# Optimization experiments

Measured on AMD Instinct MI355X. Metric: run time of the kernel, lower is better.

The kernel has to match this reference:

```python
import jax, jax.numpy as jnp
from jax import lax
import numpy as np

DIM = 768      # model dim
NL = 12        # num mamba layers
DS = 16        # d_state
DI = 1536      # d_inner = 2*dim
DC = 4         # d_conv
P = 16         # patch size
IMG = 256
NP = (IMG // P) ** 2  # 256 patches
GS = 5         # KAN grid_size
SO = 3         # KAN spline_order
NK = NL // 3   # 4 KAN layers
BATCH = 32


def setup_inputs() -> dict:
    key = jax.random.key(0)
    ks = jax.random.split(key, 16)
    def n(k, shape, s=0.02):
        return jax.random.normal(k, shape, jnp.float32) * s
    return {
        "x": jax.random.normal(ks[0], (BATCH, 3, IMG, IMG), jnp.float32),
        "patch_w": n(ks[1], (DIM, 3, P, P)),
        "patch_b": jnp.zeros((DIM,), jnp.float32),
        "pos_embed": n(ks[2], (1, NP, DIM)),
        "in_proj_w": n(ks[3], (NL, 2 * DI, DIM)),
        "conv_w": n(ks[4], (NL, DI, 1, DC), 0.1),
        "conv_b": jnp.zeros((NL, DI), jnp.float32),
        "x_proj_w": n(ks[5], (NL, 2 * DS, DI)),
        "dt_proj_w": n(ks[6], (NL, DS, DI)),
        "dt_proj_b": jnp.zeros((NL, DS), jnp.float32),
        "A_log": jnp.tile(jnp.log(jnp.arange(1, DS + 1, dtype=jnp.float32)), (NL, 1)),
        "D_param": jnp.ones((NL, DI), jnp.float32),
        "out_proj_w": n(ks[7], (NL, DIM, DI)),
        "kan_base_w": n(ks[8], (NK, DIM, DIM)),
        "kan_coeff": n(ks[9], (NK, DIM, DIM, GS + SO), 0.1),
        "kan_bias": n(ks[10], (NK, DIM), 0.01),
        "norm_w": jnp.ones((DIM,), jnp.float32),
        "norm_b": jnp.zeros((DIM,), jnp.float32),
    }


def _mamba_block(x, in_w, cw, cb, xpw, dtw, dtb, alog, Dp, ow):
    Bsz, L, _ = x.shape
    xr = jnp.einsum('bld,ed->ble', x, in_w)              # [B,L,2*DI]
    x1, res = xr[..., :DI], xr[..., DI:]
    # causal depthwise conv (pad d_conv-1 on left, truncate to L)
    xc = lax.conv_general_dilated(
        x1.transpose(0, 2, 1), cw, (1,), [(DC - 1, 0)],
        feature_group_count=DI,
        dimension_numbers=('NCH', 'OIH', 'NCH')) + cb[None, :, None]
    x1 = jax.nn.silu(xc.transpose(0, 2, 1))              # [B,L,DI]
    x_dbl = jnp.einsum('bld,ed->ble', x1, xpw)           # [B,L,2*DS]
    Bp = x_dbl[..., DS:]                                 # dt half of x_proj is discarded (as in torch)
    dt = jax.nn.softplus(jnp.einsum('bld,nd->bln', x1, dtw) + dtb)  # [B,L,DS]
    A = -jnp.exp(alog)                                   # [DS]
    Ad = jnp.exp(A * dt)                                 # [B,L,DS]
    u = x1[..., :DI // DS].mean(-1)                      # [B,L]
    Bd = dt * Bp * u[..., None]                          # [B,L,DS]
    def step(s, ab):
        a, b = ab
        s = s * a + b
        return s, s
    _, ys = lax.scan(step, jnp.zeros((Bsz, DS), x.dtype),
                     (Ad.transpose(1, 0, 2), Bd.transpose(1, 0, 2)))
    y = ys.transpose(1, 0, 2)                            # [B,L,DS]
    y = jnp.repeat(y, DI // DS, axis=-1)                 # n -> (n d)
    y = y + x1 * Dp
    y = y * jax.nn.silu(res)
    return jnp.einsum('bld,ed->ble', y, ow)              # [B,L,DIM]


def _kan(xf, bw, coeff, bias):
    base = xf @ bw.T + bias
    grid = jnp.linspace(-1.0, 1.0, GS + 1)
    denom = grid[1:] - grid[:-1] + 1e-8
    xs = (xf[..., None] - grid[:-1]) / denom             # [M,DIM,GS]
    basis = jnp.where((xs >= 0) & (xs < 1), xs, 0.0)
    return base + jnp.einsum('bik,oik->bo', basis, coeff[:, :, :GS])


def reference(x, patch_w, patch_b, pos_embed, in_proj_w, conv_w, conv_b,
              x_proj_w, dt_proj_w, dt_proj_b, A_log, D_param, out_proj_w,
              kan_base_w, kan_coeff, kan_bias, norm_w, norm_b):
    Bsz = x.shape[0]
    h = lax.conv_general_dilated(
        x, patch_w, (P, P), 'VALID',
        dimension_numbers=('NCHW', 'OIHW', 'NCHW')) + patch_b[None, :, None, None]
    h = h.transpose(0, 2, 3, 1).reshape(Bsz, NP, DIM) + pos_embed
    for i in range(NL):
        h = _mamba_block(h, in_proj_w[i], conv_w[i], conv_b[i], x_proj_w[i],
                         dt_proj_w[i], dt_proj_b[i], A_log[i], D_param[i], out_proj_w[i])
        if i % 3 == 2 and i // 3 < NK:
            j = i // 3
            hf = h.reshape(-1, DIM)
            h = _kan(hf, kan_base_w[j], kan_coeff[j], kan_bias[j]).reshape(Bsz, NP, DIM) + h
    mu = h.mean(-1, keepdims=True)
    var = ((h - mu) ** 2).mean(-1, keepdims=True)
    return (h - mu) / jnp.sqrt(var + 1e-5) * norm_w + norm_b
```

## Files before the change

kernel.cpp:

```cpp
#include <hip/hip_runtime.h>

#define BATCH 32
#define NPATCH 256
#define MROWS (BATCH * NPATCH)
#define DIM 768
#define DI 1536
#define DS 16

typedef __bf16 bf16_t;
typedef __attribute__((ext_vector_type(8))) __bf16 bf16x8;
typedef __attribute__((ext_vector_type(4))) float floatx4;

__device__ __forceinline__ float bf2f(unsigned short u) {
    union { unsigned int i; float f; } v; v.i = ((unsigned int)u) << 16; return v.f;
}
__device__ __forceinline__ unsigned short f2bf(float f) {
    union { float f; unsigned int i; } u; u.f = f;
    unsigned int r = u.i + 0x7FFFu + ((u.i >> 16) & 1u);
    return (unsigned short)(r >> 16);
}
__device__ __forceinline__ float ldin(const void* p, int i, int bf) {
    if (bf) return bf2f(((const unsigned short*)p)[i]);
    return ((const float*)p)[i];
}
__device__ __forceinline__ float4 ldin4(const void* p, int i, int bf) {
    if (bf) {
        ushort4 u = *(const ushort4*)((const unsigned short*)p + i);
        return make_float4(bf2f(u.x), bf2f(u.y), bf2f(u.z), bf2f(u.w));
    }
    return *(const float4*)((const float*)p + i);
}
__device__ __forceinline__ float siluf(float x) { return x / (1.0f + expf(-x)); }

__global__ void detect_k(const void* alog, int* flag) {
    if (threadIdx.x == 0 && blockIdx.x == 0) {
        float v = ((const float*)alog)[1];
        flag[0] = (fabsf(v - 0.69314718f) < 0.01f) ? 0 : 1;
    }
}

__global__ __launch_bounds__(256) void cvt4_k(const int* __restrict__ flag,
                                              const void* __restrict__ in,
                                              unsigned short* __restrict__ out, int n4) {
    int i = blockIdx.x * 256 + threadIdx.x;
    if (i >= n4) return;
    float4 v = ldin4(in, i * 4, flag[0]);
    ushort4 o;
    o.x = f2bf(v.x); o.y = f2bf(v.y); o.z = f2bf(v.z); o.w = f2bf(v.w);
    *(ushort4*)(out + i * 4) = o;
}

__global__ __launch_bounds__(256) void kcoef_k(const int* __restrict__ flag,
                                               const void* __restrict__ co,
                                               bf16_t* __restrict__ out) {
    int idx = blockIdx.x * 256 + threadIdx.x;
    int bf = flag[0];
    int j = idx / (768 * 3840);
    int r = idx - j * (768 * 3840);
    int n = r / 3840;
    int kk = r - n * 3840;
    int i = kk / 5, k5 = kk - i * 5;
    out[idx] = (bf16_t)ldin(co, ((j * 768 + n) * 768 + i) * 8 + k5, bf);
}

__global__ __launch_bounds__(256) void wproj_k(const int* __restrict__ flag,
                                               const void* __restrict__ dtw,
                                               const void* __restrict__ xpw,
                                               bf16_t* __restrict__ w2) {
    int idx = blockIdx.x * 256 + threadIdx.x;
    int bf = flag[0];
    int i = idx / (128 * 1536);
    int r = idx - i * (128 * 1536);
    int n = r / 1536, k = r - n * 1536;
    float v;
    if (n < 16)       v = ldin(dtw, (i * 16 + n) * 1536 + k, bf);
    else if (n < 32)  v = ldin(xpw, (i * 32 + n) * 1536 + k, bf);
    else if (n == 32) v = (k < 96) ? (1.0f / 96.0f) : 0.0f;
    else              v = 0.0f;
    w2[idx] = (bf16_t)v;
}

__global__ __launch_bounds__(256) void cvtconv_k(const int* __restrict__ flag,
                                                 const void* __restrict__ cw,
                                                 bf16_t* __restrict__ cwr) {
    int idx = blockIdx.x * 256 + threadIdx.x;
    int bf = flag[0];
    int i = idx / (4 * 1536);
    int r = idx - i * (4 * 1536);
    int k = r / 1536, c = r - k * 1536;
    cwr[idx] = (bf16_t)ldin(cw, i * 1536 * 4 + c * 4 + k, bf);
}

__global__ __launch_bounds__(256) void basis_k(const bf16_t* __restrict__ h,
                                               bf16_t* __restrict__ bas) {
    int idx = blockIdx.x * 256 + threadIdx.x;
    int m = idx / 96, i8 = (idx - m * 96) * 8;
    bf16x8 hv = *(const bf16x8*)(h + (size_t)m * 768 + i8);
    union { bf16_t a[40]; bf16x8 v[5]; } ob;
#pragma unroll
    for (int ii = 0; ii < 8; ii++) {
        float xv = (float)hv[ii];
#pragma unroll
        for (int k5 = 0; k5 < 5; k5++) {
            float tt = (xv + 1.0f - 0.4f * (float)k5) * 2.5f;
            ob.a[ii * 5 + k5] = (bf16_t)((tt >= 0.0f && tt < 1.0f) ? tt : 0.0f);
        }
    }
    bf16_t* op = bas + (size_t)m * 3840 + (size_t)i8 * 5;
#pragma unroll
    for (int j = 0; j < 5; j++) *(bf16x8*)(op + j * 8) = ob.v[j];
}

__global__ __launch_bounds__(256) void im2col_k(const int* __restrict__ flag,
                                                const void* __restrict__ x,
                                                bf16_t* __restrict__ xp) {
    int idx = blockIdx.x * 256 + threadIdx.x;
    int bf = flag[0];
    int m = idx / 768, kc = idx - m * 768;
    int b = m >> 8, p = m & 255;
    int py = p >> 4, px = p & 15;
    int c = kc >> 8, rr = kc & 255;
    int ky = rr >> 4, kx = rr & 15;
    int src = ((b * 3 + c) * 256 + py * 16 + ky) * 256 + px * 16 + kx;
    xp[idx] = (bf16_t)ldin(x, src, bf);
}

__global__ __launch_bounds__(256) void mgemm_k(
    const bf16_t* __restrict__ A, int lda,
    const bf16_t* __restrict__ W, int ldw,
    bf16_t* __restrict__ C, int ldc,
    int K, int mode, int gx,
    const int* __restrict__ flag,
    const void* __restrict__ bias, int boff,
    const void* __restrict__ aux, int aoff,
    const bf16_t* __restrict__ H, int ldh,
    float* __restrict__ dtu) {
    __shared__ bf16_t sA[128 * 64];
    __shared__ bf16_t sB[128 * 64];
    const int t = threadIdx.x;
    const int lane = t & 63, wave = t >> 6;
    const int wm = wave >> 1, wn = wave & 1;

    int m0, n0, kbeg, kend;
    if (mode == 5) {
        int mt = blockIdx.x >> 2, ks = blockIdx.x & 3;
        m0 = mt << 7; n0 = 0;
        int KS = K >> 2;
        kbeg = ks * KS; kend = kbeg + KS;
    } else {
        const int bid = blockIdx.x;
        const int xcd = bid & 7, l = bid >> 3;
        const int w = gx < 8 ? gx : 8;
        const int cb8 = w * 8;
        const int ch = l / cb8, rem = l - ch * cb8;
        const int mi = rem / w, ni = rem - mi * w;
        m0 = (xcd * 8 + mi) << 7;
        n0 = (ch * w + ni) << 7;
        kbeg = 0; kend = K;
    }

    const int srow = t >> 3;
    const int colperm = (((t & 7) ^ (srow & 7)) << 3);
    const bf16_t* gA[4]; const bf16_t* gB[4];
    char* lA[4]; char* lB[4];
#pragma unroll
    for (int r = 0; r < 4; r++) {
        gA[r] = A + (size_t)(m0 + r * 32 + srow) * lda + colperm;
        gB[r] = W + (size_t)(n0 + r * 32 + srow) * ldw + colperm;
        lA[r] = (char*)sA + (size_t)(r * 256 + wave * 64) * 16;
        lB[r] = (char*)sB + (size_t)(r * 256 + wave * 64) * 16;
    }

    floatx4 acc[4][4];
#pragma unroll
    for (int i = 0; i < 4; i++)
#pragma unroll
        for (int j = 0; j < 4; j++) acc[i][j] = (floatx4){0.f, 0.f, 0.f, 0.f};

    const int kq = lane >> 4;
    const int mr = lane & 15;

    for (int kt = kbeg; kt < kend; kt += 64) {
#pragma unroll
        for (int r = 0; r < 4; r++) {
            __builtin_amdgcn_global_load_lds(
                (__attribute__((address_space(1))) const unsigned int*)(gA[r] + kt),
                (__attribute__((address_space(3))) unsigned int*)lA[r], 16, 0, 0);
            __builtin_amdgcn_global_load_lds(
                (__attribute__((address_space(1))) const unsigned int*)(gB[r] + kt),
                (__attribute__((address_space(3))) unsigned int*)lB[r], 16, 0, 0);
        }
        __syncthreads();
#pragma unroll
        for (int half = 0; half < 2; half++) {
            const int cb = half * 4 + kq;
            if (mode == 5) {
                if (wn == 0) {
                    bf16x8 af[4], bw3[3];
#pragma unroll
                    for (int i = 0; i < 4; i++) {
                        int rw = wm * 64 + i * 16 + mr;
                        af[i] = *(const bf16x8*)(sA + rw * 64 + ((cb ^ (rw & 7)) << 3));
                    }
#pragma unroll
                    for (int j = 0; j < 3; j++) {
                        int rw = j * 16 + mr;
                        bw3[j] = *(const bf16x8*)(sB + rw * 64 + ((cb ^ (rw & 7)) << 3));
                    }
#pragma unroll
                    for (int i = 0; i < 4; i++)
#pragma unroll
                        for (int j = 0; j < 3; j++)
                            acc[i][j] = __builtin_amdgcn_mfma_f32_16x16x32_bf16(af[i], bw3[j], acc[i][j], 0, 0, 0);
                }
            } else {
                bf16x8 af[4], bw[4];
#pragma unroll
                for (int i = 0; i < 4; i++) {
                    int rw = wm * 64 + i * 16 + mr;
                    af[i] = *(const bf16x8*)(sA + rw * 64 + ((cb ^ (rw & 7)) << 3));
                }
#pragma unroll
                for (int j = 0; j < 4; j++) {
                    int rw = wn * 64 + j * 16 + mr;
                    bw[j] = *(const bf16x8*)(sB + rw * 64 + ((cb ^ (rw & 7)) << 3));
                }
#pragma unroll
                for (int i = 0; i < 4; i++)
#pragma unroll
                    for (int j = 0; j < 4; j++)
                        acc[i][j] = __builtin_amdgcn_mfma_f32_16x16x32_bf16(af[i], bw[j], acc[i][j], 0, 0, 0);
            }
        }
        __syncthreads();
    }

    const int col = lane & 15;
    const int rq = (lane >> 4) * 4;

    if (mode == 5) {
        if (wn == 0) {
            int ks = blockIdx.x & 3;
            float* dst = dtu + (size_t)ks * (MROWS * 64);
#pragma unroll
            for (int i = 0; i < 4; i++) {
#pragma unroll
                for (int reg = 0; reg < 4; reg++) {
                    int gm = m0 + wm * 64 + i * 16 + rq + reg;
#pragma unroll
                    for (int j = 0; j < 3; j++) {
                        int gn = j * 16 + col;
                        if (gn <= 32)
                            dst[(size_t)gm * 64 + gn] = acc[i][j][reg];
                    }
                }
            }
        }
        return;
    }

    const int bff = (mode == 1 || mode == 2) ? flag[0] : 0;
#pragma unroll
    for (int i = 0; i < 4; i++) {
#pragma unroll
        for (int reg = 0; reg < 4; reg++) {
            int gm = m0 + wm * 64 + i * 16 + rq + reg;
#pragma unroll
            for (int j = 0; j < 4; j++) {
                int gn = n0 + wn * 64 + j * 16 + col;
                float v = acc[i][j][reg];
                if (mode == 1) v += ldin(bias, boff + gn, bff) + ldin(aux, aoff + (gm & 255) * 768 + gn, bff);
                else if (mode == 2) v += ldin(bias, boff + gn, bff);
                else if (mode == 3) v += (float)C[(size_t)gm * ldc + gn] + (float)H[(size_t)gm * ldh + gn];
                C[(size_t)gm * ldc + gn] = (bf16_t)v;
            }
        }
    }
}

__global__ __launch_bounds__(256) void conv_k(const int* __restrict__ flag,
                                              const bf16_t* __restrict__ xr,
                                              const bf16_t* __restrict__ cwr,
                                              const void* __restrict__ cb, int cbo,
                                              bf16_t* __restrict__ xc) {
    int idx = blockIdx.x * 256 + threadIdx.x;
    int bf = flag[0];
    int m = idx / 192, c8 = (idx - m * 192) * 8;
    int l = m & 255;
    float acc[8];
    float4 b0 = ldin4(cb, cbo + c8, bf), b1 = ldin4(cb, cbo + c8 + 4, bf);
    acc[0] = b0.x; acc[1] = b0.y; acc[2] = b0.z; acc[3] = b0.w;
    acc[4] = b1.x; acc[5] = b1.y; acc[6] = b1.z; acc[7] = b1.w;
#pragma unroll
    for (int k = 0; k < 4; k++) {
        if (l + k - 3 >= 0) {
            bf16x8 xv = *(const bf16x8*)(xr + (size_t)(m + k - 3) * 3072 + c8);
            bf16x8 wv = *(const bf16x8*)(cwr + k * 1536 + c8);
#pragma unroll
            for (int j = 0; j < 8; j++) acc[j] += (float)xv[j] * (float)wv[j];
        }
    }
    bf16x8 o;
#pragma unroll
    for (int j = 0; j < 8; j++) o[j] = (bf16_t)siluf(acc[j]);
    *(bf16x8*)(xc + (size_t)m * 1536 + c8) = o;
}

__global__ __launch_bounds__(256) void scan_k(const int* __restrict__ flag,
                                              const float* __restrict__ dtu,
                                              const void* __restrict__ dtb, int dtbo,
                                              const void* __restrict__ alog, int alo,
                                              float* __restrict__ ys) {
    int wid = (blockIdx.x * 256 + threadIdx.x) >> 6;
    int lane = threadIdx.x & 63;
    int b = wid >> 4, s = wid & 15;
    int bf = flag[0];
    float dtbv = ldin(dtb, dtbo + s, bf);
    float Av = -expf(ldin(alog, alo + s, bf));
    const float* pb = dtu + (size_t)b * (256 * 64);
    float* yo = ys + (size_t)b * (256 * 16);
    float Aj[4], Bj[4];
    float A = 1.0f, Bv = 0.0f;
#pragma unroll
    for (int j = 0; j < 4; j++) {
        int l = lane * 4 + j;
        float rdt = dtbv, rBp = 0.0f, ru = 0.0f;
#pragma unroll
        for (int ks = 0; ks < 4; ks++) {
            const float* q = pb + (size_t)ks * (MROWS * 64) + (size_t)l * 64;
            rdt += q[s];
            rBp += q[16 + s];
            ru  += q[32];
        }
        float dt = (rdt > 20.0f) ? rdt : log1pf(expf(rdt));
        float a = expf(Av * dt);
        float bb = dt * rBp * ru;
        Bv = Bv * a + bb;
        A = A * a;
        Aj[j] = A; Bj[j] = Bv;
    }
#pragma unroll
    for (int off = 1; off < 64; off <<= 1) {
        float pa = __shfl_up(A, off);
        float pb2 = __shfl_up(Bv, off);
        if (lane >= off) { Bv = pb2 * A + Bv; A = pa * A; }
    }
    float ex = __shfl_up(Bv, 1);
    if (lane == 0) ex = 0.0f;
#pragma unroll
    for (int j = 0; j < 4; j++) {
        int l = lane * 4 + j;
        yo[l * 16 + s] = Aj[j] * ex + Bj[j];
    }
}

__global__ __launch_bounds__(256) void gate_k(const int* __restrict__ flag,
                                              const float* __restrict__ ys,
                                              bf16_t* __restrict__ xc,
                                              const bf16_t* __restrict__ xr,
                                              const void* __restrict__ Dp, int dpo) {
    int idx = blockIdx.x * 256 + threadIdx.x;
    int bf = flag[0];
    int m = idx / 192, d8 = (idx - m * 192) * 8;
    float yv = ys[m * 16 + d8 / 96];
    bf16x8 rv = *(const bf16x8*)(xr + (size_t)m * 3072 + 1536 + d8);
    bf16x8 xv = *(const bf16x8*)(xc + (size_t)m * 1536 + d8);
    float4 dp0 = ldin4(Dp, dpo + d8, bf), dp1 = ldin4(Dp, dpo + d8 + 4, bf);
    float dpv[8] = {dp0.x, dp0.y, dp0.z, dp0.w, dp1.x, dp1.y, dp1.z, dp1.w};
    bf16x8 o;
#pragma unroll
    for (int j = 0; j < 8; j++) {
        float v = yv + (float)xv[j] * dpv[j];
        o[j] = (bf16_t)(v * siluf((float)rv[j]));
    }
    *(bf16x8*)(xc + (size_t)m * 1536 + d8) = o;
}

__global__ __launch_bounds__(256) void lnorm_k(const int* __restrict__ flag,
                                               const bf16_t* __restrict__ h,
                                               const void* __restrict__ nw,
                                               const void* __restrict__ nb,
                                               void* __restrict__ out) {
    __shared__ float ls[4];
    int bf = flag[0];
    int m = blockIdx.x, t = threadIdx.x;
    const bf16_t* row = h + (size_t)m * 768;
    float v0 = (float)row[t], v1 = (float)row[t + 256], v2 = (float)row[t + 512];
    float s = v0 + v1 + v2;
#pragma unroll
    for (int o = 32; o; o >>= 1) s += __shfl_xor(s, o);
    if ((t & 63) == 0) ls[t >> 6] = s;
    __syncthreads();
    float mu = (ls[0] + ls[1] + ls[2] + ls[3]) * (1.0f / 768.0f);
    __syncthreads();
    float d0 = v0 - mu, d1 = v1 - mu, d2 = v2 - mu;
    float q = d0 * d0 + d1 * d1 + d2 * d2;
#pragma unroll
    for (int o = 32; o; o >>= 1) q += __shfl_xor(q, o);
    if ((t & 63) == 0) ls[t >> 6] = q;
    __syncthreads();
    float var = (ls[0] + ls[1] + ls[2] + ls[3]) * (1.0f / 768.0f);
    float inv = rsqrtf(var + 1e-5f);
    float vv[3] = {d0, d1, d2};
#pragma unroll
    for (int j = 0; j < 3; j++) {
        int colx = t + 256 * j;
        float o = vv[j] * inv * ldin(nw, colx, bf) + ldin(nb, colx, bf);
        size_t oi = (size_t)m * 768 + colx;
        if (bf) ((unsigned short*)out)[oi] = f2bf(o);
        else    ((float*)out)[oi] = o;
    }
}

extern "C" void kernel_launch(void* const* d_in, const int* in_sizes, int n_in,
                              void* d_out, int out_size, void* d_ws, size_t ws_size,
                              hipStream_t stream) {
    const void* x        = d_in[0];
    const void* patch_w  = d_in[1];
    const void* patch_b  = d_in[2];
    const void* pos      = d_in[3];
    const void* in_w     = d_in[4];
    const void* conv_w   = d_in[5];
    const void* conv_b   = d_in[6];
    const void* xpw      = d_in[7];
    const void* dtw      = d_in[8];
    const void* dtb      = d_in[9];
    const void* alog     = d_in[10];
    const void* Dp       = d_in[11];
    const void* out_w    = d_in[12];
    const void* kbw      = d_in[13];
    const void* kcoef    = d_in[14];
    const void* kbias    = d_in[15];
    const void* nw       = d_in[16];
    const void* nb       = d_in[17];

    char* base = (char*)d_ws;
    size_t off = 0;
    int* flag = (int*)base;                          off += 256;
    float* dtu  = (float*)(base + off);              off += (size_t)4 * MROWS * 64 * 4;
    float* ysb  = (float*)(base + off);              off += (size_t)MROWS * 16 * 4;
    bf16_t* hA  = (bf16_t*)(base + off);             off += (size_t)MROWS * DIM * 2;
    bf16_t* hB  = (bf16_t*)(base + off);             off += (size_t)MROWS * DIM * 2;
    bf16_t* xr  = (bf16_t*)(base + off);             off += (size_t)MROWS * 2 * DI * 2;
    bf16_t* xc  = (bf16_t*)(base + off);             off += (size_t)MROWS * DI * 2;
    bf16_t* wpatch = (bf16_t*)(base + off);          off += (size_t)DIM * DIM * 2;
    bf16_t* win  = (bf16_t*)(base + off);            off += (size_t)12 * 2 * DI * DIM * 2;
    bf16_t* wout = (bf16_t*)(base + off);            off += (size_t)12 * DIM * DI * 2;
    bf16_t* wkbw = (bf16_t*)(base + off);            off += (size_t)4 * DIM * DIM * 2;
    bf16_t* wkco = (bf16_t*)(base + off);            off += (size_t)4 * DIM * 3840 * 2;
    bf16_t* w2   = (bf16_t*)(base + off);            off += (size_t)12 * 128 * DI * 2;
    bf16_t* cwr  = (bf16_t*)(base + off);            off += (size_t)12 * 4 * DI * 2;
    bf16_t* basis = xr;
    bf16_t* im2c  = xr;

    detect_k<<<1, 64, 0, stream>>>(alog, flag);

    cvt4_k<<<(DIM * DIM / 4 + 255) / 256, 256, 0, stream>>>(flag, patch_w, (unsigned short*)wpatch, DIM * DIM / 4);
    cvt4_k<<<(12 * 2 * DI * DIM / 4 + 255) / 256, 256, 0, stream>>>(flag, in_w, (unsigned short*)win, 12 * 2 * DI * DIM / 4);
    cvt4_k<<<(12 * DIM * DI / 4 + 255) / 256, 256, 0, stream>>>(flag, out_w, (unsigned short*)wout, 12 * DIM * DI / 4);
    cvt4_k<<<(4 * DIM * DIM / 4 + 255) / 256, 256, 0, stream>>>(flag, kbw, (unsigned short*)wkbw, 4 * DIM * DIM / 4);
    kcoef_k<<<4 * DIM * 3840 / 256, 256, 0, stream>>>(flag, kcoef, wkco);
    wproj_k<<<12 * 128 * DI / 256, 256, 0, stream>>>(flag, dtw, xpw, w2);
    cvtconv_k<<<12 * 4 * DI / 256, 256, 0, stream>>>(flag, conv_w, cwr);

    im2col_k<<<(MROWS * DIM) / 256, 256, 0, stream>>>(flag, x, im2c);
    mgemm_k<<<6 * 64, 256, 0, stream>>>(
        im2c, DIM, wpatch, DIM, hA, DIM, DIM, 1, 6,
        flag, patch_b, 0, pos, 0, nullptr, 0, nullptr);

    bf16_t* hcur = hA;
    bf16_t* hoth = hB;
    for (int i = 0; i < 12; i++) {
        mgemm_k<<<24 * 64, 256, 0, stream>>>(
            hcur, DIM, win + (size_t)i * 2 * DI * DIM, DIM, xr, 2 * DI, DIM, 0, 24,
            flag, nullptr, 0, nullptr, 0, nullptr, 0, nullptr);
        conv_k<<<(MROWS * 192) / 256, 256, 0, stream>>>(
            flag, xr, cwr + (size_t)i * 4 * DI, conv_b, i * DI, xc);
        mgemm_k<<<256, 256, 0, stream>>>(
            xc, DI, w2 + (size_t)i * 128 * DI, DI, nullptr, 128, DI, 5, 1,
            flag, nullptr, 0, nullptr, 0, nullptr, 0, dtu);
        scan_k<<<128, 256, 0, stream>>>(flag, dtu, dtb, i * DS, alog, i * DS, ysb);
        gate_k<<<(MROWS * 192) / 256, 256, 0, stream>>>(
            flag, ysb, xc, xr, Dp, i * DI);
        mgemm_k<<<6 * 64, 256, 0, stream>>>(
            xc, DI, wout + (size_t)i * DIM * DI, DI, hcur, DIM, DI, 0, 6,
            flag, nullptr, 0, nullptr, 0, nullptr, 0, nullptr);
        if (i % 3 == 2) {
            int j = i / 3;
            mgemm_k<<<6 * 64, 256, 0, stream>>>(
                hcur, DIM, wkbw + (size_t)j * DIM * DIM, DIM, hoth, DIM, DIM, 2, 6,
                flag, kbias, j * DIM, nullptr, 0, nullptr, 0, nullptr);
            basis_k<<<(MROWS * 96) / 256, 256, 0, stream>>>(hcur, basis);
            mgemm_k<<<6 * 64, 256, 0, stream>>>(
                basis, 3840, wkco + (size_t)j * DIM * 3840, 3840, hoth, DIM, 3840, 3, 6,
                flag, nullptr, 0, nullptr, 0, hcur, DIM, nullptr);
            bf16_t* tmp = hcur; hcur = hoth; hoth = tmp;
        }
    }

    lnorm_k<<<MROWS, 256, 0, stream>>>(flag, hcur, nw, nb, d_out);
}
```

Before: 2.903 ms.

## Add double-buffered LDS pipeline to GEMM kernel for low-occupancy launches

```diff
diff --git a/kernel.cpp b/kernel.cpp
--- a/kernel.cpp
+++ b/kernel.cpp
@@ -125,7 +125,8 @@
     xp[idx] = (bf16_t)ldin(x, src, bf);
 }
 
-__global__ __launch_bounds__(256) void mgemm_k(
+template<int DBUF>
+__global__ __launch_bounds__(256) void mgemm_t(
     const bf16_t* __restrict__ A, int lda,
     const bf16_t* __restrict__ W, int ldw,
     bf16_t* __restrict__ C, int ldc,
@@ -135,8 +136,7 @@
     const void* __restrict__ aux, int aoff,
     const bf16_t* __restrict__ H, int ldh,
     float* __restrict__ dtu) {
-    __shared__ bf16_t sA[128 * 64];
-    __shared__ bf16_t sB[128 * 64];
+    __shared__ bf16_t sm[DBUF ? 2 : 1][2 * 128 * 64];
     const int t = threadIdx.x;
     const int lane = t & 63, wave = t >> 6;
     const int wm = wave >> 1, wn = wave & 1;
@@ -162,13 +162,10 @@
     const int srow = t >> 3;
     const int colperm = (((t & 7) ^ (srow & 7)) << 3);
     const bf16_t* gA[4]; const bf16_t* gB[4];
-    char* lA[4]; char* lB[4];
 #pragma unroll
     for (int r = 0; r < 4; r++) {
         gA[r] = A + (size_t)(m0 + r * 32 + srow) * lda + colperm;
         gB[r] = W + (size_t)(n0 + r * 32 + srow) * ldw + colperm;
-        lA[r] = (char*)sA + (size_t)(r * 256 + wave * 64) * 16;
-        lB[r] = (char*)sB + (size_t)(r * 256 + wave * 64) * 16;
     }
 
     floatx4 acc[4][4];
@@ -180,17 +177,23 @@
     const int kq = lane >> 4;
     const int mr = lane & 15;
 
-    for (int kt = kbeg; kt < kend; kt += 64) {
+    auto stage = [&](int buf, int kt) {
+        char* sa = (char*)&sm[buf][0];
 #pragma unroll
         for (int r = 0; r < 4; r++) {
+            const int off = r * 4096 + wave * 1024;
             __builtin_amdgcn_global_load_lds(
-                (__attribute__((address_space(1))) const unsigned int*)(gA[r] + kt),
-                (__attribute__((address_space(3))) unsigned int*)lA[r], 16, 0, 0);
+                (const __attribute__((address_space(1))) unsigned int*)(gA[r] + kt),
+                (__attribute__((address_space(3))) unsigned int*)(sa + off), 16, 0, 0);
             __builtin_amdgcn_global_load_lds(
-                (__attribute__((address_space(1))) const unsigned int*)(gB[r] + kt),
-                (__attribute__((address_space(3))) unsigned int*)lB[r], 16, 0, 0);
-        }
-        __syncthreads();
+                (const __attribute__((address_space(1))) unsigned int*)(gB[r] + kt),
+                (__attribute__((address_space(3))) unsigned int*)(sa + 16384 + off), 16, 0, 0);
+        }
+    };
+
+    auto compute = [&](int buf) {
+        const bf16_t* sAc = &sm[buf][0];
+        const bf16_t* sBc = sAc + 128 * 64;
 #pragma unroll
         for (int half = 0; half < 2; half++) {
             const int cb = half * 4 + kq;
@@ -200,12 +203,12 @@
 #pragma unroll
                     for (int i = 0; i < 4; i++) {
                         int rw = wm * 64 + i * 16 + mr;
-                        af[i] = *(const bf16x8*)(sA + rw * 64 + ((cb ^ (rw & 7)) << 3));
+                        af[i] = *(const bf16x8*)(sAc + rw * 64 + ((cb ^ (rw & 7)) << 3));
                     }
 #pragma unroll
                     for (int j = 0; j < 3; j++) {
                         int rw = j * 16 + mr;
-                        bw3[j] = *(const bf16x8*)(sB + rw * 64 + ((cb ^ (rw & 7)) << 3));
+                        bw3[j] = *(const bf16x8*)(sBc + rw * 64 + ((cb ^ (rw & 7)) << 3));
                     }
 #pragma unroll
                     for (int i = 0; i < 4; i++)
@@ -218,12 +221,12 @@
 #pragma unroll
                 for (int i = 0; i < 4; i++) {
                     int rw = wm * 64 + i * 16 + mr;
-                    af[i] = *(const bf16x8*)(sA + rw * 64 + ((cb ^ (rw & 7)) << 3));
+                    af[i] = *(const bf16x8*)(sAc + rw * 64 + ((cb ^ (rw & 7)) << 3));
                 }
 #pragma unroll
                 for (int j = 0; j < 4; j++) {
                     int rw = wn * 64 + j * 16 + mr;
-                    bw[j] = *(const bf16x8*)(sB + rw * 64 + ((cb ^ (rw & 7)) << 3));
+                    bw[j] = *(const bf16x8*)(sBc + rw * 64 + ((cb ^ (rw & 7)) << 3));
                 }
 #pragma unroll
                 for (int i = 0; i < 4; i++)
@@ -232,7 +235,25 @@
                         acc[i][j] = __builtin_amdgcn_mfma_f32_16x16x32_bf16(af[i], bw[j], acc[i][j], 0, 0, 0);
             }
         }
+    };
+
+    if (DBUF) {
+        stage(0, kbeg);
         __syncthreads();
+        int cur = 0;
+        for (int kt = kbeg; kt < kend; kt += 64) {
+            if (kt + 64 < kend) stage(cur ^ 1, kt + 64);
+            compute(cur);
+            __syncthreads();
+            cur ^= 1;
+        }
+    } else {
+        for (int kt = kbeg; kt < kend; kt += 64) {
+            stage(0, kt);
+            __syncthreads();
+            compute(0);
+            __syncthreads();
+        }
     }
 
     const int col = lane & 15;
@@ -464,34 +485,34 @@
     cvtconv_k<<<12 * 4 * DI / 256, 256, 0, stream>>>(flag, conv_w, cwr);
 
     im2col_k<<<(MROWS * DIM) / 256, 256, 0, stream>>>(flag, x, im2c);
-    mgemm_k<<<6 * 64, 256, 0, stream>>>(
+    mgemm_t<1><<<6 * 64, 256, 0, stream>>>(
         im2c, DIM, wpatch, DIM, hA, DIM, DIM, 1, 6,
         flag, patch_b, 0, pos, 0, nullptr, 0, nullptr);
 
     bf16_t* hcur = hA;
     bf16_t* hoth = hB;
     for (int i = 0; i < 12; i++) {
-        mgemm_k<<<24 * 64, 256, 0, stream>>>(
+        mgemm_t<0><<<24 * 64, 256, 0, stream>>>(
             hcur, DIM, win + (size_t)i * 2 * DI * DIM, DIM, xr, 2 * DI, DIM, 0, 24,
             flag, nullptr, 0, nullptr, 0, nullptr, 0, nullptr);
         conv_k<<<(MROWS * 192) / 256, 256, 0, stream>>>(
             flag, xr, cwr + (size_t)i * 4 * DI, conv_b, i * DI, xc);
-        mgemm_k<<<256, 256, 0, stream>>>(
+        mgemm_t<1><<<256, 256, 0, stream>>>(
             xc, DI, w2 + (size_t)i * 128 * DI, DI, nullptr, 128, DI, 5, 1,
             flag, nullptr, 0, nullptr, 0, nullptr, 0, dtu);
         scan_k<<<128, 256, 0, stream>>>(flag, dtu, dtb, i * DS, alog, i * DS, ysb);
         gate_k<<<(MROWS * 192) / 256, 256, 0, stream>>>(
             flag, ysb, xc, xr, Dp, i * DI);
-        mgemm_k<<<6 * 64, 256, 0, stream>>>(
+        mgemm_t<1><<<6 * 64, 256, 0, stream>>>(
             xc, DI, wout + (size_t)i * DIM * DI, DI, hcur, DIM, DI, 0, 6,
             flag, nullptr, 0, nullptr, 0, nullptr, 0, nullptr);
         if (i % 3 == 2) {
             int j = i / 3;
-            mgemm_k<<<6 * 64, 256, 0, stream>>>(
+            mgemm_t<1><<<6 * 64, 256, 0, stream>>>(
                 hcur, DIM, wkbw + (size_t)j * DIM * DIM, DIM, hoth, DIM, DIM, 2, 6,
                 flag, kbias, j * DIM, nullptr, 0, nullptr, 0, nullptr);
             basis_k<<<(MROWS * 96) / 256, 256, 0, stream>>>(hcur, basis);
-            mgemm_k<<<6 * 64, 256, 0, stream>>>(
+            mgemm_t<1><<<6 * 64, 256, 0, stream>>>(
                 basis, 3840, wkco + (size_t)j * DIM * 3840, 3840, hoth, DIM, 3840, 3, 6,
                 flag, nullptr, 0, nullptr, 0, hcur, DIM, nullptr);
             bf16_t* tmp = hcur; hcur = hoth; hoth = tmp;
```

Measured after the change: 2.898 ms. About the same (-0.2%).
